# Performance work log

Hardware: AMD Instinct MI355X
Metric: run time of the kernel (lower is better)

The kernel has to match this reference:

```python
import jax, jax.numpy as jnp
import numpy as np

NUM_HEADS = 32
NUM_KV_HEADS = 8
HEAD_DIM = 128
SCALE = 0.08838834764831845  # head_dim ** -0.5
LENS = [1024, 900, 800, 700, 600, 500, 400, 300]  # ragged sequence lengths


def setup_inputs() -> dict:
    key = jax.random.key(0)
    kq, kk, kv = jax.random.split(key, 3)
    cu = np.concatenate([[0], np.cumsum(LENS)]).astype(np.int32)
    T = int(cu[-1])  # 5224 total tokens
    q = jax.random.normal(kq, (T, NUM_HEADS * HEAD_DIM), jnp.float32)
    k = jax.random.normal(kk, (T, NUM_KV_HEADS * HEAD_DIM), jnp.float32)
    v = jax.random.normal(kv, (T, NUM_KV_HEADS * HEAD_DIM), jnp.float32)
    return {"q": q, "k": k, "v": v, "cu_seqlens": jnp.asarray(cu), "max_seqlen": 1024}


def _varlen_indices(cu_seqlens, total_tokens):
    # For each flat token, which sequence it belongs to and its position within it.
    pos = jnp.arange(total_tokens)
    seq_idx = jnp.searchsorted(cu_seqlens[1:], pos, side='right')
    pos_idx = pos - cu_seqlens[seq_idx]
    return seq_idx, pos_idx


def reference(q, k, v, cu_seqlens, max_seqlen):
    T = q.shape[0]
    B = cu_seqlens.shape[0] - 1
    q = q.reshape(T, NUM_HEADS, HEAD_DIM)
    k = k.reshape(T, NUM_KV_HEADS, HEAD_DIM)
    v = v.reshape(T, NUM_KV_HEADS, HEAD_DIM)
    si, pi = _varlen_indices(cu_seqlens, T)

    # varlen -> padded [B, L, H, D] (scatter)
    def pad(x):
        return jnp.zeros((B, max_seqlen) + x.shape[1:], x.dtype).at[si, pi].set(x)

    qp, kp, vp = pad(q), pad(k), pad(v)

    # GQA: repeat_interleave KV heads to match query heads
    rep = NUM_HEADS // NUM_KV_HEADS
    kp = jnp.repeat(kp, rep, axis=2)
    vp = jnp.repeat(vp, rep, axis=2)

    # causal SDPA on padded tensors
    scores = jnp.einsum('bihd,bjhd->bhij', qp, kp) * SCALE  # [B,H,L,L]
    causal = jnp.tril(jnp.ones((max_seqlen, max_seqlen), bool))
    scores = jnp.where(causal, scores, -jnp.inf)
    attn = jax.nn.softmax(scores, axis=-1)
    op = jnp.einsum('bhij,bjhd->bihd', attn, vp)  # [B,L,H,D]

    # padded -> varlen [T, H, D] (gather)
    return op[si, pi]
```

## Files before the change

kernel.cpp:

```cpp
#include <hip/hip_runtime.h>
#include <math.h>

#define NUM_HEADS 32
#define NUM_KV_HEADS 8
#define HEAD_DIM 128
#define QSTRIDE 4096
#define KSTRIDE 1024
#define SCALE 0.08838834764831845f
#define BM 128
#define PSP 72
#define K1C (SCALE * 1.4426950408889634f)
#define K2C (6.0f * 1.4426950408889634f)

typedef __attribute__((ext_vector_type(8))) short short8;
typedef __attribute__((ext_vector_type(16))) float floatx16;
typedef __attribute__((ext_vector_type(4))) float f32x4;

__constant__ unsigned char PERM41[41] = {
  7, 15, 6, 14, 21, 5, 13, 20, 26, 31, 4, 12, 19, 25, 35, 30,
  3, 11, 18, 24, 34, 38, 29, 2, 10, 17, 23, 33, 37, 40, 28,
  1, 9, 16, 22, 32, 36, 39, 27, 0, 8};

__device__ __forceinline__ ushort f2bf(float f) {
  union { float f; unsigned u; } x; x.f = f;
  unsigned r = x.u + 0x7fffu + ((x.u >> 16) & 1u);
  return (ushort)(r >> 16);
}

__device__ __forceinline__ unsigned cvtpk(float lo, float hi) {
  unsigned r;
  asm("v_cvt_pk_bf16_f32 %0, %1, %2" : "=v"(r) : "v"(lo), "v"(hi));
  return r;
}

__global__ __launch_bounds__(256)
void prep(const float* __restrict__ k, const float* __restrict__ v,
          ushort* __restrict__ kfr, ushort* __restrict__ vfr,
          int T, int NB32, int NB16) {
  const int kt = (int)blockIdx.x * 64;
  const int kvh = (int)blockIdx.y;
  __shared__ __align__(16) ushort Kt[64][136];
  __shared__ __align__(16) ushort Vs[128][PSP];
  {
    const int key = threadIdx.x >> 2;
    const int dc = (threadIdx.x & 3) * 32;
    const bool inb = (kt + key) < T;
    const float* gk = k + (size_t)(kt + key) * KSTRIDE + kvh * HEAD_DIM + dc;
    const float* gv = v + (size_t)(kt + key) * KSTRIDE + kvh * HEAD_DIM + dc;
    #pragma unroll
    for (int i = 0; i < 32; i += 8) {
      float4 a = inb ? *(const float4*)(gk + i) : make_float4(0.f, 0.f, 0.f, 0.f);
      float4 b = inb ? *(const float4*)(gk + i + 4) : make_float4(0.f, 0.f, 0.f, 0.f);
      ushort w[8] = {f2bf(a.x), f2bf(a.y), f2bf(a.z), f2bf(a.w),
                     f2bf(b.x), f2bf(b.y), f2bf(b.z), f2bf(b.w)};
      *(short8*)&Kt[key][dc + i] = *(short8*)w;
    }
    #pragma unroll
    for (int i = 0; i < 32; i += 4) {
      float4 x = inb ? *(const float4*)(gv + i) : make_float4(0.f, 0.f, 0.f, 0.f);
      Vs[dc + i + 0][key] = f2bf(x.x);
      Vs[dc + i + 1][key] = f2bf(x.y);
      Vs[dc + i + 2][key] = f2bf(x.z);
      Vs[dc + i + 3][key] = f2bf(x.w);
    }
  }
  __syncthreads();
  const int l = threadIdx.x & 63;
  const int wv = threadIdx.x >> 6;
  const int l32 = l & 31;
  const int hb = l >> 5;
  #pragma unroll
  for (int q0 = 0; q0 < 4; q0++) {
    int c = q0 * 4 + wv;
    int kb2 = c >> 3, s = c & 7;
    short8 d = *(const short8*)&Kt[kb2 * 32 + l32][s * 16 + hb * 8];
    *(short8*)(kfr + ((size_t)(kvh * NB32 + (kt >> 5) + kb2) * 8 + s) * 512 + l * 8) = d;
  }
  #pragma unroll
  for (int q0 = 0; q0 < 4; q0++) {
    int c = q0 * 4 + wv;
    int kb = c >> 2, i = c & 3;
    short8 d = *(const short8*)&Vs[i * 32 + l32][kb * 16 + hb * 8];
    *(short8*)(vfr + ((size_t)(kvh * NB16 + (kt >> 4) + kb) * 4 + i) * 512 + l * 8) = d;
  }
}

__global__ __launch_bounds__(256, 2)
void fa_kernel(const float* __restrict__ q, const ushort* __restrict__ kfr,
               const ushort* __restrict__ vfr, const int* __restrict__ cu,
               float* __restrict__ out, int T, int NB32, int NB16, int B, int nt) {
  const int tid = threadIdx.x;
  const int wave = tid >> 6;
  const int lane = tid & 63;
  const int l32 = lane & 31;
  const int half = lane >> 5;
  const int h = ((int)blockIdx.x & 7) * 4 + ((int)blockIdx.x >> 3);
  const int kvh = h >> 2;
  const int tile = (nt == 41) ? (int)PERM41[blockIdx.y] : (nt - 1 - (int)blockIdx.y);
  const int row0 = tile * BM;
  const int myrow = row0 + wave * 32 + l32;

  int rs_q = 0, tk_q = -1;
  if (myrow < T) {
    int s = 0;
    while (s < B - 1 && cu[s + 1] <= myrow) s++;
    rs_q = cu[s]; tk_q = myrow;
  }
  int s0 = 0;
  while (s0 < B - 1 && cu[s0 + 1] <= row0) s0++;
  const int kt0 = (cu[s0] / 32) * 32;
  const int tmax = min(row0 + BM - 1, T - 1);

  short8 aq[8];
  if (myrow < T) {
    const float* gq = q + (size_t)myrow * QSTRIDE + h * HEAD_DIM + half * 8;
    #pragma unroll
    for (int s = 0; s < 8; s++) {
      f32x4 x = __builtin_nontemporal_load((const f32x4*)(gq + s * 16));
      f32x4 y = __builtin_nontemporal_load((const f32x4*)(gq + s * 16 + 4));
      ushort w[8] = {f2bf(x.x), f2bf(x.y), f2bf(x.z), f2bf(x.w),
                     f2bf(y.x), f2bf(y.y), f2bf(y.z), f2bf(y.w)};
      aq[s] = *(short8*)w;
    }
  } else {
    #pragma unroll
    for (int s = 0; s < 8; s++) aq[s] = (short8){0, 0, 0, 0, 0, 0, 0, 0};
  }

  const ushort* kbase = kfr + (size_t)kvh * NB32 * 4096 + lane * 8;
  const ushort* vbase = vfr + (size_t)kvh * NB16 * 2048 + lane * 8;

  short8 kf[8];
  {
    const ushort* kp = kbase + (size_t)(kt0 >> 5) * 4096;
    #pragma unroll
    for (int s = 0; s < 8; s++) kf[s] = *(const short8*)(kp + s * 512);
  }

  floatx16 o0 = {0.f,0.f,0.f,0.f,0.f,0.f,0.f,0.f,0.f,0.f,0.f,0.f,0.f,0.f,0.f,0.f};
  floatx16 o1 = o0, o2 = o0, o3 = o0;
  float sm = 0.f;

  for (int kt = kt0; kt <= tmax; kt += 32) {
    short8 vf[8];
    {
      const ushort* vp = vbase + (size_t)(kt >> 4) * 2048;
      #pragma unroll
      for (int c = 0; c < 8; c++) vf[c] = *(const short8*)(vp + c * 512);
    }

    floatx16 ca = {0.f,0.f,0.f,0.f,0.f,0.f,0.f,0.f,0.f,0.f,0.f,0.f,0.f,0.f,0.f,0.f};
    floatx16 cb = ca;
    __builtin_amdgcn_s_setprio(1);
    #pragma unroll
    for (int s = 0; s < 8; s += 2) {
      ca = __builtin_amdgcn_mfma_f32_32x32x16_bf16(kf[s], aq[s], ca, 0, 0, 0);
      cb = __builtin_amdgcn_mfma_f32_32x32x16_bf16(kf[s + 1], aq[s + 1], cb, 0, 0, 0);
    }
    __builtin_amdgcn_s_setprio(0);

    {
      int ktn = kt + 32;
      const ushort* kp = kbase + (size_t)(((ktn <= tmax) ? ktn : kt0) >> 5) * 4096;
      #pragma unroll
      for (int s = 0; s < 8; s++) kf[s] = *(const short8*)(kp + s * 512);
    }

    const bool fullt = __all((rs_q <= kt) & (tk_q >= kt + 31));
    if (fullt) {
      #pragma unroll
      for (int r = 0; r < 16; r++) {
        ca[r] = __builtin_amdgcn_exp2f(fmaf(ca[r] + cb[r], K1C, -K2C));
        sm += ca[r];
      }
    } else {
      #pragma unroll
      for (int r = 0; r < 16; r++) {
        int key = kt + (r & 3) + 8 * (r >> 2) + 4 * half;
        bool vld = (key >= rs_q) & (key <= tk_q);
        ca[r] = vld ? __builtin_amdgcn_exp2f(fmaf(ca[r] + cb[r], K1C, -K2C)) : 0.f;
        sm += ca[r];
      }
    }

    #pragma unroll
    for (int g = 0; g < 2; g++) {
      const int r0 = g * 8;
      unsigned w0 = cvtpk(ca[r0 + 0], ca[r0 + 1]);
      unsigned w1 = cvtpk(ca[r0 + 2], ca[r0 + 3]);
      unsigned w2 = cvtpk(ca[r0 + 4], ca[r0 + 5]);
      unsigned w3 = cvtpk(ca[r0 + 6], ca[r0 + 7]);
      asm("v_permlane32_swap_b32 %0, %1" : "+v"(w0), "+v"(w2));
      asm("v_permlane32_swap_b32 %0, %1" : "+v"(w1), "+v"(w3));
      union { unsigned u[4]; short8 s8; } ap;
      ap.u[0] = w0; ap.u[1] = w1; ap.u[2] = w2; ap.u[3] = w3;
      o0 = __builtin_amdgcn_mfma_f32_32x32x16_bf16(ap.s8, vf[g * 4 + 0], o0, 0, 0, 0);
      o1 = __builtin_amdgcn_mfma_f32_32x32x16_bf16(ap.s8, vf[g * 4 + 1], o1, 0, 0, 0);
      o2 = __builtin_amdgcn_mfma_f32_32x32x16_bf16(ap.s8, vf[g * 4 + 2], o2, 0, 0, 0);
      o3 = __builtin_amdgcn_mfma_f32_32x32x16_bf16(ap.s8, vf[g * 4 + 3], o3, 0, 0, 0);
    }
  }

  float smT = sm + __shfl_xor(sm, 32, 64);
  #pragma unroll
  for (int r = 0; r < 16; r++) {
    int qr = (r & 3) + 8 * (r >> 2) + 4 * half;
    float dn = __shfl(smT, qr, 64);
    int tkr = __shfl(tk_q, qr, 64);
    if (tkr >= 0) {
      float inv = 1.f / dn;
      float* go = out + (size_t)tkr * QSTRIDE + h * HEAD_DIM + l32;
      __builtin_nontemporal_store(o0[r] * inv, go);
      __builtin_nontemporal_store(o1[r] * inv, go + 32);
      __builtin_nontemporal_store(o2[r] * inv, go + 64);
      __builtin_nontemporal_store(o3[r] * inv, go + 96);
    }
  }
}

extern "C" void kernel_launch(void* const* d_in, const int* in_sizes, int n_in,
                              void* d_out, int out_size, void* d_ws, size_t ws_size,
                              hipStream_t stream) {
  const float* q = (const float*)d_in[0];
  const float* k = (const float*)d_in[1];
  const float* v = (const float*)d_in[2];
  const int* cu = (const int*)d_in[3];
  float* out = (float*)d_out;
  int T = in_sizes[0] / QSTRIDE;
  int B = in_sizes[3] - 1;
  int Tpad = ((T + 63) / 64) * 64;
  int NB32 = Tpad / 32, NB16 = Tpad / 16;

  ushort* kfr = (ushort*)d_ws;
  ushort* vfr = kfr + (size_t)Tpad * 1024;

  hipLaunchKernelGGL(prep, dim3(Tpad / 64, NUM_KV_HEADS), dim3(256), 0, stream,
                     k, v, kfr, vfr, T, NB32, NB16);
  int nt = (T + BM - 1) / BM;
  hipLaunchKernelGGL(fa_kernel, dim3(NUM_HEADS, nt), dim3(256), 0, stream,
                     q, kfr, vfr, cu, out, T, NB32, NB16, B, nt);
}
```

Measured before the change: 251.8 us.

## Use per-wave key ranges and prefetch V fragments a tile ahead

Each wave now computes its own key start (from its first row's sequence start) and end (its own last row) instead of sharing the block-wide range, so waves skip key tiles that are fully masked for their 32 rows. V fragments are also loaded for the next tile after the PV MFMAs, giving the V loads a whole iteration to arrive, in the same way K was already prefetched. Waves within a block now run different trip counts, which can unbalance them, and holding the prefetched V values adds register pressure.

```diff
diff --git a/kernel.cpp b/kernel.cpp
--- a/kernel.cpp
+++ b/kernel.cpp
@@ -98,7 +98,8 @@
   const int kvh = h >> 2;
   const int tile = (nt == 41) ? (int)PERM41[blockIdx.y] : (nt - 1 - (int)blockIdx.y);
   const int row0 = tile * BM;
-  const int myrow = row0 + wave * 32 + l32;
+  const int wrow0 = row0 + wave * 32;
+  const int myrow = wrow0 + l32;
 
   int rs_q = 0, tk_q = -1;
   if (myrow < T) {
@@ -106,10 +107,8 @@
     while (s < B - 1 && cu[s + 1] <= myrow) s++;
     rs_q = cu[s]; tk_q = myrow;
   }
-  int s0 = 0;
-  while (s0 < B - 1 && cu[s0 + 1] <= row0) s0++;
-  const int kt0 = (cu[s0] / 32) * 32;
-  const int tmax = min(row0 + BM - 1, T - 1);
+  const int wkt0 = (__shfl(rs_q, 0, 64) / 32) * 32;
+  const int wtmax = (wrow0 < T) ? min(wrow0 + 31, T - 1) : -1;
 
   short8 aq[8];
   if (myrow < T) {
@@ -127,28 +126,20 @@
     for (int s = 0; s < 8; s++) aq[s] = (short8){0, 0, 0, 0, 0, 0, 0, 0};
   }
 
-  const ushort* kbase = kfr + (size_t)kvh * NB32 * 4096 + lane * 8;
-  const ushort* vbase = vfr + (size_t)kvh * NB16 * 2048 + lane * 8;
-
-  short8 kf[8];
-  {
-    const ushort* kp = kbase + (size_t)(kt0 >> 5) * 4096;
-    #pragma unroll
-    for (int s = 0; s < 8; s++) kf[s] = *(const short8*)(kp + s * 512);
-  }
+  const ushort* kp = kfr + (size_t)kvh * NB32 * 4096 + (size_t)(wkt0 >> 5) * 4096 + lane * 8;
+  const ushort* vp = vfr + (size_t)kvh * NB16 * 2048 + (size_t)(wkt0 >> 4) * 2048 + lane * 8;
+
+  short8 kf[8], vf[8];
+  #pragma unroll
+  for (int s = 0; s < 8; s++) kf[s] = *(const short8*)(kp + s * 512);
+  #pragma unroll
+  for (int c = 0; c < 8; c++) vf[c] = *(const short8*)(vp + c * 512);
 
   floatx16 o0 = {0.f,0.f,0.f,0.f,0.f,0.f,0.f,0.f,0.f,0.f,0.f,0.f,0.f,0.f,0.f,0.f};
   floatx16 o1 = o0, o2 = o0, o3 = o0;
   float sm = 0.f;
 
-  for (int kt = kt0; kt <= tmax; kt += 32) {
-    short8 vf[8];
-    {
-      const ushort* vp = vbase + (size_t)(kt >> 4) * 2048;
-      #pragma unroll
-      for (int c = 0; c < 8; c++) vf[c] = *(const short8*)(vp + c * 512);
-    }
-
+  for (int kt = wkt0; kt <= wtmax; kt += 32) {
     floatx16 ca = {0.f,0.f,0.f,0.f,0.f,0.f,0.f,0.f,0.f,0.f,0.f,0.f,0.f,0.f,0.f,0.f};
     floatx16 cb = ca;
     __builtin_amdgcn_s_setprio(1);
@@ -159,12 +150,10 @@
     }
     __builtin_amdgcn_s_setprio(0);
 
-    {
-      int ktn = kt + 32;
-      const ushort* kp = kbase + (size_t)(((ktn <= tmax) ? ktn : kt0) >> 5) * 4096;
-      #pragma unroll
-      for (int s = 0; s < 8; s++) kf[s] = *(const short8*)(kp + s * 512);
-    }
+    const bool more = (kt + 32) <= wtmax;
+    kp += more ? 4096 : 0;
+    #pragma unroll
+    for (int s = 0; s < 8; s++) kf[s] = *(const short8*)(kp + s * 512);
 
     const bool fullt = __all((rs_q <= kt) & (tk_q >= kt + 31));
     if (fullt) {
@@ -199,6 +188,10 @@
       o2 = __builtin_amdgcn_mfma_f32_32x32x16_bf16(ap.s8, vf[g * 4 + 2], o2, 0, 0, 0);
       o3 = __builtin_amdgcn_mfma_f32_32x32x16_bf16(ap.s8, vf[g * 4 + 3], o3, 0, 0, 0);
     }
+
+    vp += more ? 4096 : 0;
+    #pragma unroll
+    for (int c = 0; c < 8; c++) vf[c] = *(const short8*)(vp + c * 512);
   }
 
   float smT = sm + __shfl_xor(sm, 32, 64);
```

Result: faster. 246.8 us (-2.0%).
